# Kernel optimization log

Measured on AMD Instinct MI355X. Metric: run time of the kernel, lower is better.

## Reference

```python
import jax, jax.numpy as jnp
import numpy as np

N_QUBITS = 10
DIM = 1 << N_QUBITS  # 1024

# Constant QFT matrix (PennyLane convention: F[j,k] = w^{jk}/sqrt(N), w = exp(2*pi*i/N),
# wire 0 = most significant bit). Symmetric, so state @ F == F @ state per sample.
_jk = (np.outer(np.arange(DIM), np.arange(DIM)) % DIM).astype(np.float64)
QFT_MAT = jnp.asarray((np.exp(2j * np.pi * _jk / DIM) / np.sqrt(DIM)).astype(np.complex64))


def _apply_1q(state, U, q):
    """Apply 2x2 gate U to wire q (wire 0 = MSB). state: [B, DIM] complex."""
    B = state.shape[0]
    left, right = 1 << q, 1 << (N_QUBITS - 1 - q)
    s = state.reshape(B, left, 2, right)
    s = jnp.einsum('ij,bajc->baic', U, s)
    return s.reshape(B, DIM)


def _apply_cnot(state, c, t):
    """CNOT with control c, target t (wire 0 = MSB)."""
    B = state.shape[0]
    a, b = (c, t) if c < t else (t, c)
    s = state.reshape(B, 1 << a, 2, 1 << (b - a - 1), 2, 1 << (N_QUBITS - 1 - b))
    ctrl_ax, tgt_ax = (2, 4) if c < t else (4, 2)
    s0 = jax.lax.index_in_dim(s, 0, ctrl_ax, keepdims=False)
    s1 = jax.lax.index_in_dim(s, 1, ctrl_ax, keepdims=False)
    ta = tgt_ax - 1 if tgt_ax > ctrl_ax else tgt_ax  # target axis after squeezing ctrl
    s1 = jnp.flip(s1, axis=ta)  # X on target when control == 1
    s = jnp.stack([s0, s1], axis=ctrl_ax)
    return s.reshape(B, DIM)


def _rx(t):
    c = jnp.cos(t / 2).astype(jnp.complex64)
    s = (-1j * jnp.sin(t / 2)).astype(jnp.complex64)
    return jnp.stack([jnp.stack([c, s]), jnp.stack([s, c])])


def _ry(t):
    c = jnp.cos(t / 2).astype(jnp.complex64)
    s = jnp.sin(t / 2).astype(jnp.complex64)
    return jnp.stack([jnp.stack([c, -s]), jnp.stack([s, c])])


def _rz(t):
    e = jnp.exp(-0.5j * t.astype(jnp.complex64))
    z = jnp.zeros((), jnp.complex64)
    return jnp.stack([jnp.stack([e, z]), jnp.stack([z, jnp.conj(e)])])


def _forward(x, weights):
    B = x.shape[0]
    # Pad/truncate is a no-op here (x already [B, DIM]); normalize as in the module.
    nrm = jnp.linalg.norm(x, axis=-1, keepdims=True)
    xn = x / jnp.maximum(nrm, 1e-8)
    state = xn.astype(jnp.complex64)  # AmplitudeEmbedding (already unit-norm)
    for q in range(N_QUBITS):
        state = _apply_1q(state, _rx(weights[q, 0]), q)
    for q in range(N_QUBITS):
        state = _apply_1q(state, _ry(weights[q, 1]), q)
    for q in range(N_QUBITS):
        state = _apply_1q(state, _rz(weights[q, 2]), q)
    for q in range(N_QUBITS):
        state = _apply_cnot(state, q, (q + 1) % N_QUBITS)
    for q in range(N_QUBITS):
        state = _apply_1q(state, _ry(weights[q, 3]), q)
    state = state @ QFT_MAT  # QFT (symmetric matrix)
    ex, ey, ez = [], [], []
    for q in range(N_QUBITS):
        s = state.reshape(B, 1 << q, 2, 1 << (N_QUBITS - 1 - q))
        s0, s1 = s[:, :, 0, :], s[:, :, 1, :]
        cross = jnp.sum(jnp.conj(s0) * s1, axis=(1, 2))
        ex.append(2.0 * jnp.real(cross))                # <X_q>
        ey.append(2.0 * jnp.imag(cross))                # <Y_q>
        ez.append(jnp.sum(jnp.abs(s0) ** 2 - jnp.abs(s1) ** 2, axis=(1, 2)))  # <Z_q>
    return jnp.stack(ex + ey + ez, axis=1).astype(jnp.float32)  # [B, 3*N_QUBITS]


def setup_inputs() -> dict:
    key = jax.random.key(0)
    kx, kw = jax.random.split(key)
    x = jax.random.normal(kx, (8192, 1024), dtype=jnp.float32)
    weights = jax.random.normal(kw, (10, 4), dtype=jnp.float32) * 0.01
    return {"x": x, "weights": weights}


def reference(x, weights):
    return _forward(x, weights)
```

## Files before the change

### kernel.cpp

```cpp
#include <hip/hip_runtime.h>


__device__ __forceinline__ float wred(float v) {
    v += __shfl_xor(v, 1);
    v += __shfl_xor(v, 2);
    v += __shfl_xor(v, 4);
    v += __shfl_xor(v, 8);
    v += __shfl_xor(v, 16);
    v += __shfl_xor(v, 32);
    return v;
}

__global__ __launch_bounds__(256) void fused_kernel(const float* __restrict__ w,
                                                    const float* __restrict__ x,
                                                    float* __restrict__ out)
{
    __shared__ float uu[10][8];
    __shared__ float ryc[10], rys[10];
    __shared__ __align__(16) float scr[4][2048];
    const int tid = threadIdx.x;
    const int wv = tid >> 6, l = tid & 63;
    const int row = blockIdx.x * 4 + wv;
    float* bw = scr[wv];

    if (tid < 10) {
        float t0 = w[tid*4 + 0] * 0.5f, t1 = w[tid*4 + 1] * 0.5f;
        float t2 = w[tid*4 + 2] * 0.5f, t3 = w[tid*4 + 3] * 0.5f;
        float s0, c0, s1, c1, s2, c2, s3, c3;
        __sincosf(t0, &s0, &c0);
        __sincosf(t1, &s1, &c1);
        __sincosf(t2, &s2, &c2);
        __sincosf(t3, &s3, &c3);
        uu[tid][0] =  c2*c1*c0 + s2*s1*s0;
        uu[tid][1] =  c2*s1*s0 - s2*c1*c0;
        uu[tid][2] = -(c2*s1*c0 + s2*c1*s0);
        uu[tid][3] =  s2*s1*c0 - c2*c1*s0;
        uu[tid][4] =  c2*s1*c0 + s2*c1*s0;
        uu[tid][5] =  s2*s1*c0 - c2*c1*s0;
        uu[tid][6] =  c2*c1*c0 + s2*s1*s0;
        uu[tid][7] =  s2*c1*c0 - c2*s1*s0;
        ryc[tid] = c3;
        rys[tid] = s3;
    }
    __syncthreads();

    const float* xr = x + (size_t)row * 1024 + l * 16;
    float4 v0 = ((const float4*)xr)[0];
    float4 v1 = ((const float4*)xr)[1];
    float4 v2 = ((const float4*)xr)[2];
    float4 v3 = ((const float4*)xr)[3];
    float ss = v0.x*v0.x + v0.y*v0.y + v0.z*v0.z + v0.w*v0.w
             + v1.x*v1.x + v1.y*v1.y + v1.z*v1.z + v1.w*v1.w
             + v2.x*v2.x + v2.y*v2.y + v2.z*v2.z + v2.w*v2.w
             + v3.x*v3.x + v3.y*v3.y + v3.z*v3.z + v3.w*v3.w;
    ss = wred(ss);
    const float scale = 0.03125f / fmaxf(sqrtf(ss), 1e-8f);

    float2 c[16];
    c[0]  = make_float2(v0.x*scale, 0.f); c[1]  = make_float2(v0.y*scale, 0.f);
    c[2]  = make_float2(v0.z*scale, 0.f); c[3]  = make_float2(v0.w*scale, 0.f);
    c[4]  = make_float2(v1.x*scale, 0.f); c[5]  = make_float2(v1.y*scale, 0.f);
    c[6]  = make_float2(v1.z*scale, 0.f); c[7]  = make_float2(v1.w*scale, 0.f);
    c[8]  = make_float2(v2.x*scale, 0.f); c[9]  = make_float2(v2.y*scale, 0.f);
    c[10] = make_float2(v2.z*scale, 0.f); c[11] = make_float2(v2.w*scale, 0.f);
    c[12] = make_float2(v3.x*scale, 0.f); c[13] = make_float2(v3.y*scale, 0.f);
    c[14] = make_float2(v3.z*scale, 0.f); c[15] = make_float2(v3.w*scale, 0.f);

    #pragma unroll
    for (int p = 0; p < 4; ++p) {
        const float* U = uu[9 - p];
        const float u00r = U[0], u00i = U[1], u01r = U[2], u01i = U[3];
        const float u10r = U[4], u10i = U[5], u11r = U[6], u11i = U[7];
        const int m = 1 << p;
        #pragma unroll
        for (int i = 0; i < 16; ++i) {
            if (i & m) continue;
            const int j = i | m;
            const float ar = c[i].x, ai = c[i].y, br = c[j].x, bi = c[j].y;
            c[i].x = u00r*ar - u00i*ai + u01r*br - u01i*bi;
            c[i].y = u00r*ai + u00i*ar + u01r*bi + u01i*br;
            c[j].x = u10r*ar - u10i*ai + u11r*br - u11i*bi;
            c[j].y = u10r*ai + u10i*ar + u11r*bi + u11i*br;
        }
    }
    #pragma unroll
    for (int e = 0; e < 6; ++e) {
        const float* U = uu[5 - e];
        const int mybit = (l >> e) & 1;
        const float car = mybit ? U[6] : U[0];
        const float cai = mybit ? U[7] : U[1];
        const float cbr = mybit ? U[4] : U[2];
        const float cbi = mybit ? U[5] : U[3];
        #pragma unroll
        for (int i = 0; i < 16; ++i) {
            const float fr = __shfl_xor(c[i].x, 1 << e);
            const float fi = __shfl_xor(c[i].y, 1 << e);
            const float ar = c[i].x, ai = c[i].y;
            c[i].x = car*ar - cai*ai + cbr*fr - cbi*fi;
            c[i].y = car*ai + cai*ar + cbr*fi + cbi*fr;
        }
    }

    #pragma unroll
    for (int j = 0; j < 8; ++j) {
        const int su = l*8 + (j ^ (l & 7));
        ((float4*)bw)[su] = make_float4(c[2*j].x, c[2*j].y, c[2*j+1].x, c[2*j+1].y);
    }
    #pragma unroll
    for (int i = 0; i < 16; ++i) {
        const int k = l*16 + i;
        int m = (int)(__brev((unsigned)k) >> 22);
        #pragma unroll
        for (int q = 9; q >= 0; --q) {
            const int pc = (q == 9) ? 0 : 9 - q;
            const int pt = (q == 9) ? 9 : 8 - q;
            m ^= ((m >> pc) & 1) << pt;
        }
        const int lm = m >> 4, um = (m >> 1) & 7, lo = m & 1;
        const int su = lm*8 + (um ^ (lm & 7));
        c[i] = ((const float2*)bw)[su*2 + lo];
    }

    #pragma unroll
    for (int p = 0; p < 4; ++p) {
        const float cc = ryc[p], sv = rys[p];
        const int m = 1 << p;
        #pragma unroll
        for (int i = 0; i < 16; ++i) {
            if (i & m) continue;
            const int j = i | m;
            const float ar = c[i].x, ai = c[i].y, br = c[j].x, bi = c[j].y;
            c[i].x = cc*ar - sv*br;  c[i].y = cc*ai - sv*bi;
            c[j].x = sv*ar + cc*br;  c[j].y = sv*ai + cc*bi;
        }
    }
    #pragma unroll
    for (int e = 0; e < 6; ++e) {
        const float cc = ryc[4 + e], sv = rys[4 + e];
        const int mybit = (l >> e) & 1;
        const float sel = mybit ? sv : -sv;
        #pragma unroll
        for (int i = 0; i < 16; ++i) {
            const float fr = __shfl_xor(c[i].x, 1 << e);
            const float fi = __shfl_xor(c[i].y, 1 << e);
            c[i].x = cc*c[i].x + sel*fr;
            c[i].y = cc*c[i].y + sel*fi;
        }
    }

    #pragma unroll
    for (int st = 1; st <= 4; ++st) {
        const int hf = 1 << (st - 1);
        const float astep = 6.28318530717958647f / (float)(1 << st);
        #pragma unroll
        for (int i = 0; i < 16; ++i) {
            if (i & hf) continue;
            const int j = i | hf;
            float sw, cw;
            __sincosf(astep * (float)(i & (hf - 1)), &sw, &cw);
            const float tr = cw*c[j].x - sw*c[j].y;
            const float ti = cw*c[j].y + sw*c[j].x;
            const float ur = c[i].x, ui = c[i].y;
            c[i].x = ur + tr; c[i].y = ui + ti;
            c[j].x = ur - tr; c[j].y = ui - ti;
        }
    }
    #pragma unroll
    for (int e2 = 0; e2 < 6; ++e2) {
        const int st = 5 + e2;
        const float astep = 6.28318530717958647f / (float)(1 << st);
        const int mybit = (l >> e2) & 1;
        const float base = astep * 16.0f * (float)(l & ((1 << e2) - 1));
        #pragma unroll
        for (int i = 0; i < 16; ++i) {
            const float fr = __shfl_xor(c[i].x, 1 << e2);
            const float fi = __shfl_xor(c[i].y, 1 << e2);
            float sw, cw;
            __sincosf(base + astep * (float)i, &sw, &cw);
            const float zr = mybit ? c[i].x : fr;
            const float zi = mybit ? c[i].y : fi;
            const float tr = cw*zr - sw*zi;
            const float ti = cw*zi + sw*zr;
            const float ur = mybit ? fr : c[i].x;
            const float ui = mybit ? fi : c[i].y;
            c[i].x = mybit ? (ur - tr) : (ur + tr);
            c[i].y = mybit ? (ui - ti) : (ui + ti);
        }
    }

    #pragma unroll
    for (int j = 0; j < 8; ++j) {
        const int su = l*8 + (j ^ (l & 7));
        ((float4*)bw)[su] = make_float4(c[2*j].x, c[2*j].y, c[2*j+1].x, c[2*j+1].y);
    }

    float P2s = 0.f;
    #pragma unroll
    for (int i = 0; i < 16; ++i)
        P2s += c[i].x*c[i].x + c[i].y*c[i].y;

    float outv = 0.f;

    #pragma unroll
    for (int p = 0; p < 4; ++p) {
        const int m = 1 << p;
        const int q = 9 - p;
        float rr = 0.f, ii = 0.f, zz = 0.f;
        #pragma unroll
        for (int i = 0; i < 16; ++i) {
            if (i & m) continue;
            const int j = i | m;
            rr += c[i].x*c[j].x + c[i].y*c[j].y;
            ii += c[i].x*c[j].y - c[i].y*c[j].x;
            zz += (c[i].x*c[i].x + c[i].y*c[i].y) - (c[j].x*c[j].x + c[j].y*c[j].y);
        }
        rr = wred(rr);
        ii = wred(ii);
        zz = wred(zz);
        outv = (l == q)      ? 2.f*rr : outv;
        outv = (l == 10 + q) ? 2.f*ii : outv;
        outv = (l == 20 + q) ? zz     : outv;
    }

    #pragma unroll
    for (int e = 0; e < 6; ++e) {
        const int q = 5 - e;
        const int part = l ^ (1 << e);
        const int mybit = (l >> e) & 1;
        const float sgn = mybit ? -1.f : 1.f;
        const int j0 = mybit ? 4 : 0;
        float rr = 0.f, ii = 0.f;
        #pragma unroll
        for (int j = 0; j < 4; ++j) {
            const int su = part*8 + ((j0 + j) ^ (part & 7));
            const float4 f = ((const float4*)bw)[su];
            const float2 a0 = c[2*j],     a1 = c[2*j + 1];
            const float2 b0 = c[2*j + 8], b1 = c[2*j + 9];
            const float m0x = mybit ? b0.x : a0.x;
            const float m0y = mybit ? b0.y : a0.y;
            const float m1x = mybit ? b1.x : a1.x;
            const float m1y = mybit ? b1.y : a1.y;
            rr += m0x*f.x + m0y*f.y;
            ii += m0x*f.y - m0y*f.x;
            rr += m1x*f.z + m1y*f.w;
            ii += m1x*f.w - m1y*f.z;
        }
        const float rr_s = wred(rr);
        const float ii_s = wred(sgn * ii);
        const float zz_s = wred(sgn * P2s);
        outv = (l == q)      ? 2.f*rr_s : outv;
        outv = (l == 10 + q) ? 2.f*ii_s : outv;
        outv = (l == 20 + q) ? zz_s     : outv;
    }

    if (l < 30)
        out[(size_t)row * 30 + l] = outv;
}

extern "C" void kernel_launch(void* const* d_in, const int* in_sizes, int n_in,
                              void* d_out, int out_size, void* d_ws, size_t ws_size,
                              hipStream_t stream) {
    const float* x = (const float*)d_in[0];
    const float* w = (const float*)d_in[1];
    float* out = (float*)d_out;
    (void)d_ws; (void)ws_size;

    fused_kernel<<<2048, 256, 0, stream>>>(w, x, out);
}
```

Before: 157.9 us.

## Store LDS scratch in fp16, use constant and recurrence twiddles, raise occupancy

The per-wave LDS scratch buffer now holds complex amplitudes packed as fp16 pairs, which halves shared memory per block, and the launch bound asks for 5 blocks per CU. The in-register FFT stages take twiddles from constant tables instead of calling sincos. The cross-lane stages compute one base sincos and advance it with a complex-multiply recurrence, and they restructure the butterfly into a single shuffle and an FMA. The CNOT/bit-reversal index is split into a per-lane part and a per-i part. The trade-off is fp16 rounding of the stored state and drift from the twiddle recurrence, which lowers accuracy.

After: 215.1 us. 36.2% more time.

```diff
diff --git a/kernel.cpp b/kernel.cpp
--- a/kernel.cpp
+++ b/kernel.cpp
@@ -1,5 +1,16 @@
 #include <hip/hip_runtime.h>
 
+
+typedef _Float16 half2_t __attribute__((ext_vector_type(2)));
+
+__device__ __forceinline__ unsigned pk16(float a, float b) {
+    half2_t h; h[0] = (_Float16)a; h[1] = (_Float16)b;
+    return __builtin_bit_cast(unsigned, h);
+}
+__device__ __forceinline__ float2 up16(unsigned u) {
+    half2_t h = __builtin_bit_cast(half2_t, u);
+    return make_float2((float)h[0], (float)h[1]);
+}
 
 __device__ __forceinline__ float wred(float v) {
     v += __shfl_xor(v, 1);
@@ -11,17 +22,28 @@
     return v;
 }
 
-__global__ __launch_bounds__(256) void fused_kernel(const float* __restrict__ w,
-                                                    const float* __restrict__ x,
-                                                    float* __restrict__ out)
+__device__ __forceinline__ int cnotrev(int k) {
+    int m = (int)(__brev((unsigned)k) >> 22);
+    #pragma unroll
+    for (int q = 9; q >= 0; --q) {
+        const int pc = (q == 9) ? 0 : 9 - q;
+        const int pt = (q == 9) ? 9 : 8 - q;
+        m ^= ((m >> pc) & 1) << pt;
+    }
+    return m;
+}
+
+__global__ __launch_bounds__(256, 5) void fused_kernel(const float* __restrict__ w,
+                                                       const float* __restrict__ x,
+                                                       float* __restrict__ out)
 {
     __shared__ float uu[10][8];
     __shared__ float ryc[10], rys[10];
-    __shared__ __align__(16) float scr[4][2048];
+    __shared__ __align__(16) unsigned scr[4][1024];
     const int tid = threadIdx.x;
     const int wv = tid >> 6, l = tid & 63;
     const int row = blockIdx.x * 4 + wv;
-    float* bw = scr[wv];
+    unsigned* bw = scr[wv];
 
     if (tid < 10) {
         float t0 = w[tid*4 + 0] * 0.5f, t1 = w[tid*4 + 1] * 0.5f;
@@ -104,21 +126,18 @@
     #pragma unroll
     for (int j = 0; j < 8; ++j) {
         const int su = l*8 + (j ^ (l & 7));
-        ((float4*)bw)[su] = make_float4(c[2*j].x, c[2*j].y, c[2*j+1].x, c[2*j+1].y);
-    }
+        uint2 pv;
+        pv.x = pk16(c[2*j].x,     c[2*j].y);
+        pv.y = pk16(c[2*j + 1].x, c[2*j + 1].y);
+        ((uint2*)bw)[su] = pv;
+    }
+    const int mb = cnotrev(l << 4);
     #pragma unroll
     for (int i = 0; i < 16; ++i) {
-        const int k = l*16 + i;
-        int m = (int)(__brev((unsigned)k) >> 22);
-        #pragma unroll
-        for (int q = 9; q >= 0; --q) {
-            const int pc = (q == 9) ? 0 : 9 - q;
-            const int pt = (q == 9) ? 9 : 8 - q;
-            m ^= ((m >> pc) & 1) << pt;
-        }
+        const int m = mb ^ cnotrev(i);
         const int lm = m >> 4, um = (m >> 1) & 7, lo = m & 1;
-        const int su = lm*8 + (um ^ (lm & 7));
-        c[i] = ((const float2*)bw)[su*2 + lo];
+        const unsigned v = bw[(lm*8 + (um ^ (lm & 7)))*2 + lo];
+        c[i] = up16(v);
     }
 
     #pragma unroll
@@ -148,50 +167,67 @@
         }
     }
 
-    #pragma unroll
-    for (int st = 1; st <= 4; ++st) {
-        const int hf = 1 << (st - 1);
-        const float astep = 6.28318530717958647f / (float)(1 << st);
-        #pragma unroll
-        for (int i = 0; i < 16; ++i) {
-            if (i & hf) continue;
-            const int j = i | hf;
-            float sw, cw;
-            __sincosf(astep * (float)(i & (hf - 1)), &sw, &cw);
-            const float tr = cw*c[j].x - sw*c[j].y;
-            const float ti = cw*c[j].y + sw*c[j].x;
-            const float ur = c[i].x, ui = c[i].y;
-            c[i].x = ur + tr; c[i].y = ui + ti;
-            c[j].x = ur - tr; c[j].y = ui - ti;
-        }
-    }
-    #pragma unroll
-    for (int e2 = 0; e2 < 6; ++e2) {
-        const int st = 5 + e2;
-        const float astep = 6.28318530717958647f / (float)(1 << st);
-        const int mybit = (l >> e2) & 1;
-        const float base = astep * 16.0f * (float)(l & ((1 << e2) - 1));
-        #pragma unroll
-        for (int i = 0; i < 16; ++i) {
-            const float fr = __shfl_xor(c[i].x, 1 << e2);
-            const float fi = __shfl_xor(c[i].y, 1 << e2);
-            float sw, cw;
-            __sincosf(base + astep * (float)i, &sw, &cw);
-            const float zr = mybit ? c[i].x : fr;
-            const float zi = mybit ? c[i].y : fi;
-            const float tr = cw*zr - sw*zi;
-            const float ti = cw*zi + sw*zr;
-            const float ur = mybit ? fr : c[i].x;
-            const float ui = mybit ? fi : c[i].y;
-            c[i].x = mybit ? (ur - tr) : (ur + tr);
-            c[i].y = mybit ? (ui - ti) : (ui + ti);
+    {
+        const float TC8[8] = { 1.f,  0.92387953f,  0.70710678f,  0.38268343f,
+                               0.f, -0.38268343f, -0.70710678f, -0.92387953f };
+        const float TS8[8] = { 0.f,  0.38268343f,  0.70710678f,  0.92387953f,
+                               1.f,  0.92387953f,  0.70710678f,  0.38268343f };
+        #pragma unroll
+        for (int st = 1; st <= 4; ++st) {
+            const int hf = 1 << (st - 1);
+            #pragma unroll
+            for (int i = 0; i < 16; ++i) {
+                if (i & hf) continue;
+                const int j = i | hf;
+                const int tix = (i & (hf - 1)) << (4 - st);
+                const float cwv = TC8[tix], swv = TS8[tix];
+                const float tr = cwv*c[j].x - swv*c[j].y;
+                const float ti = cwv*c[j].y + swv*c[j].x;
+                const float ur = c[i].x, ui = c[i].y;
+                c[i].x = ur + tr; c[i].y = ui + ti;
+                c[j].x = ur - tr; c[j].y = ui - ti;
+            }
+        }
+    }
+    {
+        const float WC[6] = { 0.98078528f, 0.99518473f, 0.99879546f,
+                              0.99969882f, 0.99992470f, 0.99998118f };
+        const float WS[6] = { 0.19509032f, 0.09801714f, 0.04906767f,
+                              0.02454123f, 0.01227154f, 0.00613588f };
+        #pragma unroll
+        for (int e2 = 0; e2 < 6; ++e2) {
+            const int st = 5 + e2;
+            const float astep = 6.28318530717958647f / (float)(1 << st);
+            const int mybit = (l >> e2) & 1;
+            const float sel = mybit ? -1.f : 1.f;
+            const float cW = WC[e2], sW = WS[e2];
+            float cb, sb;
+            __sincosf(astep * 16.0f * (float)(l & ((1 << e2) - 1)), &sb, &cb);
+            float cw = cb, sw = sb;
+            #pragma unroll
+            for (int i = 0; i < 16; ++i) {
+                const float pr = cw*c[i].x - sw*c[i].y;
+                const float pi = cw*c[i].y + sw*c[i].x;
+                const float vr = mybit ? pr : c[i].x;
+                const float vi = mybit ? pi : c[i].y;
+                const float fr = __shfl_xor(vr, 1 << e2);
+                const float fi = __shfl_xor(vi, 1 << e2);
+                c[i].x = fmaf(sel, vr, fr);
+                c[i].y = fmaf(sel, vi, fi);
+                const float ncw = cw*cW - sw*sW;
+                sw = sw*cW + cw*sW;
+                cw = ncw;
+            }
         }
     }
 
     #pragma unroll
     for (int j = 0; j < 8; ++j) {
         const int su = l*8 + (j ^ (l & 7));
-        ((float4*)bw)[su] = make_float4(c[2*j].x, c[2*j].y, c[2*j+1].x, c[2*j+1].y);
+        uint2 pv;
+        pv.x = pk16(c[2*j].x,     c[2*j].y);
+        pv.y = pk16(c[2*j + 1].x, c[2*j + 1].y);
+        ((uint2*)bw)[su] = pv;
     }
 
     float P2s = 0.f;
@@ -233,17 +269,19 @@
         #pragma unroll
         for (int j = 0; j < 4; ++j) {
             const int su = part*8 + ((j0 + j) ^ (part & 7));
-            const float4 f = ((const float4*)bw)[su];
+            const uint2 d = ((const uint2*)bw)[su];
+            const float2 f01 = up16(d.x);
+            const float2 f23 = up16(d.y);
             const float2 a0 = c[2*j],     a1 = c[2*j + 1];
             const float2 b0 = c[2*j + 8], b1 = c[2*j + 9];
             const float m0x = mybit ? b0.x : a0.x;
             const float m0y = mybit ? b0.y : a0.y;
             const float m1x = mybit ? b1.x : a1.x;
             const float m1y = mybit ? b1.y : a1.y;
-            rr += m0x*f.x + m0y*f.y;
-            ii += m0x*f.y - m0y*f.x;
-            rr += m1x*f.z + m1y*f.w;
-            ii += m1x*f.w - m1y*f.z;
+            rr += m0x*f01.x + m0y*f01.y;
+            ii += m0x*f01.y - m0y*f01.x;
+            rr += m1x*f23.x + m1y*f23.y;
+            ii += m1x*f23.y - m1y*f23.x;
         }
         const float rr_s = wred(rr);
         const float ii_s = wred(sgn * ii);
```
